# Optimization experiments

Measured on AMD Instinct MI355X. Metric: run time of the kernel, lower is better.

The kernel has to match this reference:

```python
import jax, jax.numpy as jnp
import numpy as np
from jax import lax

B, N = 16, 2048
S0, S1, K = 256, 128, 32
EPS = 1e-5


def bn_relu(x, gamma, beta, axes):
    # training-mode BatchNorm (batch statistics) + ReLU; channel is last dim
    mean = jnp.mean(x, axis=axes, keepdims=True)
    var = jnp.var(x, axis=axes, keepdims=True)
    return jax.nn.relu((x - mean) * lax.rsqrt(var + EPS) * gamma + beta)


def fps(coords, s):
    # farthest point sampling, deterministic start at index 0. coords [B,N,3]
    b, n, _ = coords.shape
    def body(carry, _):
        dist, far = carry
        centroid = jnp.take_along_axis(coords, far[:, None, None], axis=1)  # [B,1,3]
        d = jnp.sum((coords - centroid) ** 2, axis=-1)                      # [B,N]
        dist = jnp.minimum(dist, d)
        return (dist, jnp.argmax(dist, axis=-1).astype(jnp.int32)), far
    init = (jnp.full((b, n), 1e10, coords.dtype), jnp.zeros((b,), jnp.int32))
    _, idx = lax.scan(body, init, None, length=s)
    return jnp.transpose(idx)  # [B,s]


def gather_points(pts, idx):
    # pts [B,N,C], idx [B,...] int -> [B,...,C]
    flat = idx.reshape(idx.shape[0], -1)[..., None]  # [B,M,1]
    out = jnp.take_along_axis(pts, flat, axis=1)     # [B,M,C]
    return out.reshape(*idx.shape, pts.shape[-1])


def sample_and_knn_group(s, k, coords, features):
    # coords [B,N,3], features [B,N,C] -> new_xyz [B,s,3], agg [B,s,k,2C]
    fps_idx = fps(coords, s)
    new_xyz = gather_points(coords, fps_idx)      # [B,s,3]
    center = gather_points(features, fps_idx)     # [B,s,C]
    d2 = jnp.sum((new_xyz[:, :, None, :] - coords[:, None, :, :]) ** 2, axis=-1)  # [B,s,N]
    _, knn_idx = lax.top_k(-d2, k)                # k smallest distances
    grouped = gather_points(features, knn_idx)    # [B,s,k,C]
    agg = jnp.concatenate(
        [grouped - center[:, :, None, :],
         jnp.broadcast_to(center[:, :, None, :], grouped.shape)], axis=-1)
    return new_xyz, agg


def sg_block(coords, features, s, k, w, gamma, beta):
    # conv1x1 -> BN -> ReLU -> max over k neighbors
    new_xyz, nf = sample_and_knn_group(s, k, coords, features)  # nf [B,s,k,d]
    h = jnp.einsum('bskd,od->bsko', nf, w)
    h = bn_relu(h, gamma, beta, axes=(0, 1, 2))
    return new_xyz, jnp.max(h, axis=2)  # [B,s,out]


def setup_inputs() -> dict:
    key = jax.random.key(0)
    ks = jax.random.split(key, 5)
    return {
        'x': jax.random.normal(ks[0], (B, 3, N), jnp.float32),
        'w1': jax.random.normal(ks[1], (64, 3), jnp.float32) * (1.0 / np.sqrt(3)),
        'g1': jnp.ones((64,), jnp.float32), 'b1': jnp.zeros((64,), jnp.float32),
        'w2': jax.random.normal(ks[2], (64, 64), jnp.float32) * 0.125,
        'g2': jnp.ones((64,), jnp.float32), 'b2': jnp.zeros((64,), jnp.float32),
        'w_sg0': jax.random.normal(ks[3], (128, 128), jnp.float32) * (1.0 / np.sqrt(128)),
        'g_sg0': jnp.ones((128,), jnp.float32), 'b_sg0': jnp.zeros((128,), jnp.float32),
        'w_sg1': jax.random.normal(ks[4], (256, 256), jnp.float32) * (1.0 / np.sqrt(256)),
        'g_sg1': jnp.ones((256,), jnp.float32), 'b_sg1': jnp.zeros((256,), jnp.float32),
    }


def reference(x, w1, g1, b1, w2, g2, b2, w_sg0, g_sg0, b_sg0, w_sg1, g_sg1, b_sg1):
    coords = jnp.transpose(x, (0, 2, 1))                   # [B,N,3]
    f = bn_relu(jnp.einsum('bnc,oc->bno', coords, w1), g1, b1, axes=(0, 1))  # [B,N,64]
    f = bn_relu(jnp.einsum('bnc,oc->bno', f, w2), g2, b2, axes=(0, 1))       # [B,N,64]
    xyz1, f1 = sg_block(coords, f, S0, K, w_sg0, g_sg0, b_sg0)   # [B,S0,128]
    _, f2 = sg_block(xyz1, f1, S1, K, w_sg1, g_sg1, b_sg1)       # [B,S1,256]
    return jnp.transpose(f2, (0, 2, 1))                           # [B,256,S1]
```

## Files before the change

kernel.cpp:

```cpp
#include <hip/hip_runtime.h>
#include <float.h>

#define BATCH 16
#define NPTS  2048
#define NS0   256
#define NS1   128
#define KK    32
#define EPSV  1e-5f
#define MROWS 32768.0f

__device__ __forceinline__ float sqdist(float ax,float ay,float az,float bx,float by,float bz){
  float dx=__fsub_rn(ax,bx), dy=__fsub_rn(ay,by), dz=__fsub_rn(az,bz);
  return __fadd_rn(__fadd_rn(__fmul_rn(dx,dx),__fmul_rn(dy,dy)),__fmul_rn(dz,dz));
}

template<int CTRL,int RM>
__device__ __forceinline__ float dpp_fmax_s(float x){
  int t = __builtin_amdgcn_update_dpp((int)0xFF800000, __float_as_int(x), CTRL, RM, 0xf, false);
  return fmaxf(x, __int_as_float(t));
}
template<int CTRL,int RM>
__device__ __forceinline__ float dpp_fmin_s(float x){
  int t = __builtin_amdgcn_update_dpp(0x7F800000, __float_as_int(x), CTRL, RM, 0xf, false);
  return fminf(x, __int_as_float(t));
}
template<int CTRL,int RM>
__device__ __forceinline__ unsigned dpp_umin_s(unsigned x){
  unsigned t = (unsigned)__builtin_amdgcn_update_dpp(-1, (int)x, CTRL, RM, 0xf, false);
  return t<x ? t : x;
}
__device__ __forceinline__ void wave_argmax_f32(float v, unsigned idx, float& mall, int& sel){
  float m=v;
  m=dpp_fmax_s<0x111,0xf>(m); m=dpp_fmax_s<0x112,0xf>(m); m=dpp_fmax_s<0x114,0xf>(m);
  m=dpp_fmax_s<0x118,0xf>(m); m=dpp_fmax_s<0x142,0xa>(m); m=dpp_fmax_s<0x143,0xc>(m);
  mall = __int_as_float(__builtin_amdgcn_readlane(__float_as_int(m),63));
  unsigned c = (v==mall)? idx : 0xFFFFFFFFu;
  c=dpp_umin_s<0x111,0xf>(c); c=dpp_umin_s<0x112,0xf>(c); c=dpp_umin_s<0x114,0xf>(c);
  c=dpp_umin_s<0x118,0xf>(c); c=dpp_umin_s<0x142,0xa>(c); c=dpp_umin_s<0x143,0xc>(c);
  sel = (int)(unsigned)__builtin_amdgcn_readlane((int)c,63);
}
__device__ __forceinline__ int wave_argmin_f32(float v, unsigned idx){
  float m=v;
  m=dpp_fmin_s<0x111,0xf>(m); m=dpp_fmin_s<0x112,0xf>(m); m=dpp_fmin_s<0x114,0xf>(m);
  m=dpp_fmin_s<0x118,0xf>(m); m=dpp_fmin_s<0x142,0xa>(m); m=dpp_fmin_s<0x143,0xc>(m);
  float mall = __int_as_float(__builtin_amdgcn_readlane(__float_as_int(m),63));
  unsigned c = (v==mall)? idx : 0xFFFFFFFFu;
  c=dpp_umin_s<0x111,0xf>(c); c=dpp_umin_s<0x112,0xf>(c); c=dpp_umin_s<0x114,0xf>(c);
  c=dpp_umin_s<0x118,0xf>(c); c=dpp_umin_s<0x142,0xa>(c); c=dpp_umin_s<0x143,0xc>(c);
  return (int)(unsigned)__builtin_amdgcn_readlane((int)c,63);
}


__device__ void embed1_body(int bid, const float* __restrict__ x, const float* __restrict__ w1,
                            float* __restrict__ coords, float* __restrict__ t1){
  __shared__ float w[192];
  __shared__ float xs[3][64];
  __shared__ float fin[64][65];
  int tid = threadIdx.x;
  if (tid < 192) w[tid] = w1[tid];
  int base = bid*64;
  int b = base / NPTS, n0 = base % NPTS;
  if (tid < 192){
    int ch = tid>>6, i = tid&63;
    xs[ch][i] = x[((size_t)b*3+ch)*NPTS + n0 + i];
  }
  __syncthreads();
  if (tid < 64){
    coords[(size_t)(base+tid)*3+0]=xs[0][tid];
    coords[(size_t)(base+tid)*3+1]=xs[1][tid];
    coords[(size_t)(base+tid)*3+2]=xs[2][tid];
  }
  int p = tid>>2, c0 = (tid&3)<<4;
  float cx=xs[0][p], cy=xs[1][p], cz=xs[2][p];
  #pragma unroll
  for(int j=0;j<16;j++){
    int c = c0+j;
    fin[p][c] = cx*w[c*3+0] + cy*w[c*3+1] + cz*w[c*3+2];
  }
  __syncthreads();
  for(int i=tid;i<4096;i+=256){
    int pp=i>>6, c=i&63;
    t1[(size_t)base*64 + i] = fin[pp][c];
  }
}

__device__ void wt_body(int gid, const float* __restrict__ w0, float* __restrict__ wt0,
                        const float* __restrict__ w1, float* __restrict__ wt1){
  if(gid < 128*128){
    int o = gid % 128, c = gid / 128;
    wt0[gid] = w0[o*128 + c];
  } else {
    int g2 = gid - 128*128;
    if(g2 >= 256*256) return;
    int o = g2 % 256, c = g2 / 256;
    wt1[g2] = w1[o*256 + c];
  }
}

__device__ void statsA_body(int blk, const float* __restrict__ t,
                            float* __restrict__ accS, float* __restrict__ accQ){
  int c = threadIdx.x;
  int r0 = blk*128;
  float s=0.f, q=0.f;
  for(int r=0;r<128;r++){
    float v = t[(size_t)(r0+r)*64 + c];
    s+=v; q+=v*v;
  }
  atomicAdd(accS+c, s);
  atomicAdd(accQ+c, q);
}

__device__ void embed2_body(int bid, const float* __restrict__ t1, const float* __restrict__ w2,
                            const float* __restrict__ accS, const float* __restrict__ accQ,
                            const float* __restrict__ g1, const float* __restrict__ b1,
                            float* __restrict__ t2, char* smem){
  float (*fin)[64] = (float(*)[64])smem;
  float* sm = (float*)smem + 4096;
  float* sr = sm+64; float* sg = sr+64; float* sb = sg+64;
  int tid = threadIdx.x;
  if (tid<64){
    float S=accS[tid], Q=accQ[tid];
    float m = S/MROWS, v = Q/MROWS - m*m; if(v<0.f) v=0.f;
    sm[tid]=m; sr[tid]=rsqrtf(v+EPSV); sg[tid]=g1[tid]; sb[tid]=b1[tid];
  }
  __syncthreads();
  int base = bid*64;
  for(int i=tid;i<4096;i+=256){
    int p=i>>6, c=i&63;
    float v = t1[(size_t)(base+p)*64 + c];
    v = (v - sm[c])*sr[c]*sg[c] + sb[c];
    fin[p][c] = v>0.f ? v : 0.f;
  }
  __syncthreads();
  int o = tid & 63, p0 = tid>>6;
  float acc[16];
  #pragma unroll
  for(int i=0;i<16;i++) acc[i]=0.f;
  for(int cc=0; cc<64; cc+=4){
    float4 wv = *(const float4*)(w2 + o*64 + cc);
    #pragma unroll
    for(int i=0;i<16;i++){
      float4 f4 = *(const float4*)&fin[p0 + i*4][cc];
      acc[i] += f4.x*wv.x + f4.y*wv.y + f4.z*wv.z + f4.w*wv.w;
    }
  }
  #pragma unroll
  for(int i=0;i<16;i++) t2[(size_t)(base+p0+i*4)*64 + o] = acc[i];
}

template<int P, int S, int T>
__device__ void fps_body(int b, const float* __restrict__ x, int* __restrict__ outIdx,
                         float* __restrict__ outXyz, char* smem){
  constexpr int PPT = P/T;
  constexpr int NW  = T/64;
  float* sx=(float*)smem; float* sy=sx+P; float* sz=sy+P;
  int* sidx=(int*)(sz+P);
  unsigned long long* rv64=(unsigned long long*)(sidx+S);
  int tid = threadIdx.x;
  const float* xb = x + (size_t)b*3*P;
  float px[PPT], py[PPT], pz[PPT], dist[PPT];
  #pragma unroll
  for(int i=0;i<PPT;i++){
    int n = i*T + tid;
    float X=xb[n], Y=xb[P+n], Z=xb[2*P+n];
    px[i]=X; py[i]=Y; pz[i]=Z; dist[i]=1e10f;
    sx[n]=X; sy[n]=Y; sz[n]=Z;
  }
  __syncthreads();
  int cur = 0;
  float cx=sx[0], cy=sy[0], cz=sz[0];
  for(int s=0;s<S;s++){
    if(tid==0) sidx[s]=cur;
    if(s==S-1) break;
    float bv=-FLT_MAX; int bi=0;
    #pragma unroll
    for(int i=0;i<PPT;i++){
      float d = sqdist(px[i],py[i],pz[i],cx,cy,cz);
      float nd = fminf(dist[i], d);
      dist[i]=nd;
      int n = i*T + tid;
      if(nd>bv){ bv=nd; bi=n; }
    }
    float mall; int sel;
    wave_argmax_f32(bv,(unsigned)bi,mall,sel);
    int sl = s & 1;
    if((tid&63)==0) rv64[sl*NW+(tid>>6)] = ((unsigned long long)__float_as_uint(mall)<<32)|(unsigned)(~sel);
    __syncthreads();
    unsigned long long wk = rv64[sl*NW];
    #pragma unroll
    for(int w=1;w<NW;w++){ unsigned long long t = rv64[sl*NW+w]; if(t>wk) wk=t; }
    cur = (int)(~(unsigned)wk);
    cx=sx[cur]; cy=sy[cur]; cz=sz[cur];
  }
  __syncthreads();
  for(int i=tid; i<S; i+=T){
    int id = sidx[i];
    outIdx[b*S+i] = id;
    outXyz[((size_t)b*S+i)*3+0] = sx[id];
    outXyz[((size_t)b*S+i)*3+1] = sy[id];
    outXyz[((size_t)b*S+i)*3+2] = sz[id];
  }
}

template<int P, int S>
__device__ void fps_wave_body(int b, const float* __restrict__ pts, int* __restrict__ outIdx,
                              float* __restrict__ outXyz, char* smem){
  constexpr int PPT = P/64;
  float4* sp = (float4*)smem;
  int* sidx = (int*)(smem + P*sizeof(float4));
  int lane = threadIdx.x;
  const float* p = pts + (size_t)b*P*3;
  float px[PPT], py[PPT], pz[PPT], dist[PPT];
  #pragma unroll
  for(int i=0;i<PPT;i++){
    int n = i*64 + lane;
    float X=p[n*3], Y=p[n*3+1], Z=p[n*3+2];
    px[i]=X; py[i]=Y; pz[i]=Z; dist[i]=1e10f;
    sp[n] = make_float4(X,Y,Z,0.f);
  }
  __syncthreads();
  int cur = 0;
  float cx=sp[0].x, cy=sp[0].y, cz=sp[0].z;
  for(int s=0;s<S;s++){
    if(lane==0) sidx[s]=cur;
    if(s==S-1) break;
    float bv=-FLT_MAX; int bi=0;
    #pragma unroll
    for(int i=0;i<PPT;i++){
      float d = sqdist(px[i],py[i],pz[i],cx,cy,cz);
      float nd = fminf(dist[i], d);
      dist[i]=nd;
      int n = i*64 + lane;
      if(nd>bv){ bv=nd; bi=n; }
    }
    float mall; int sel;
    wave_argmax_f32(bv,(unsigned)bi,mall,sel);
    cur = sel;
    float4 cp = sp[cur];
    cx=cp.x; cy=cp.y; cz=cp.z;
  }
  __syncthreads();
  for(int i=lane; i<S; i+=64){
    int id = sidx[i];
    float4 cp = sp[id];
    outIdx[b*S+i] = id;
    outXyz[((size_t)b*S+i)*3+0] = cp.x;
    outXyz[((size_t)b*S+i)*3+1] = cp.y;
    outXyz[((size_t)b*S+i)*3+2] = cp.z;
  }
}

template<int P>
__device__ void knn_body(int bq, const float* __restrict__ pts, const float* __restrict__ q,
                         int S, int* __restrict__ knn){
  constexpr int E = P/64;
  int lane = threadIdx.x;
  int b = bq / S;
  const float* p = pts + (size_t)b*P*3;
  float qx=q[(size_t)bq*3], qy=q[(size_t)bq*3+1], qz=q[(size_t)bq*3+2];
  float dl[E];
  float mv = FLT_MAX; unsigned mi = 0xFFFFFFFFu;
  #pragma unroll
  for(int i=0;i<E;i++){
    int n = i*64 + lane;
    float v = sqdist(qx,qy,qz,p[n*3],p[n*3+1],p[n*3+2]);
    dl[i] = v;
    if(v<mv){ mv=v; mi=(unsigned)n; }
  }
  for(int j=0;j<KK;j++){
    int sel = wave_argmin_f32(mv, mi);
    if(lane==0) knn[(size_t)bq*KK+j] = sel;
    if((sel & 63) == lane){
      int slot = sel >> 6;
      #pragma unroll
      for(int i=0;i<E;i++) if(i==slot) dl[i]=FLT_MAX;
      mv = FLT_MAX; mi = 0xFFFFFFFFu;
      #pragma unroll
      for(int i=0;i<E;i++){
        int n=i*64+lane;
        if(dl[i]<mv){ mv=dl[i]; mi=(unsigned)n; }
      }
    }
  }
}

template<int C, int P, bool BN>
__device__ void pass1_body(int bq, const float* __restrict__ feats, const int* __restrict__ knn,
                           const int* __restrict__ fpsIdx, const float* __restrict__ WT,
                           float* __restrict__ hmax, float* __restrict__ hmin,
                           float* __restrict__ part, int S,
                           const float* __restrict__ accS, const float* __restrict__ accQ,
                           const float* __restrict__ bg, const float* __restrict__ bb){
  constexpr int O   = 2*C;
  constexpr int TPB = C;
  constexpr int C4  = C/4;
  constexpr int OG  = O/8;
  constexpr int LDC = C+4;
  __shared__ __align__(16) float gfp[KK*LDC];
  __shared__ __align__(16) float cf[C];
  __shared__ __align__(16) float sa[BN?C:1], sbb[BN?C:1];
  __shared__ float sct[O];
  int tid = threadIdx.x;
  int b = bq / S;
  const float* fb = feats + (size_t)b*P*C;
  int ci = fpsIdx[bq];
  const float* cfg = fb + (size_t)ci*C;
  if(BN){
    float S_=accS[tid], Q_=accQ[tid];
    float m = S_/MROWS, vv = Q_/MROWS - m*m; if(vv<0.f) vv=0.f;
    float a = rsqrtf(vv+EPSV)*bg[tid];
    float sh = bb[tid] - m*a;
    sa[tid]=a; sbb[tid]=sh;
    float cv = a*cfg[tid] + sh;
    cf[tid] = cv>0.f ? cv : 0.f;
    __syncthreads();
  } else {
    cf[tid] = cfg[tid];
  }
  for(int i=tid; i<KK*C4; i+=TPB){
    int k = i/C4, d4 = i - k*C4;
    float4 g = ((const float4*)(fb + (size_t)knn[(size_t)bq*KK+k]*C))[d4];
    float4 r;
    if(BN){
      float4 a4 = *(const float4*)&sa[d4*4];
      float4 s4 = *(const float4*)&sbb[d4*4];
      float4 c4 = *(const float4*)&cf[d4*4];
      float gx = a4.x*g.x+s4.x; gx = gx>0.f?gx:0.f;
      float gy = a4.y*g.y+s4.y; gy = gy>0.f?gy:0.f;
      float gz = a4.z*g.z+s4.z; gz = gz>0.f?gz:0.f;
      float gw = a4.w*g.w+s4.w; gw = gw>0.f?gw:0.f;
      r.x=gx-c4.x; r.y=gy-c4.y; r.z=gz-c4.z; r.w=gw-c4.w;
    } else {
      float4 c4 = ((const float4*)cfg)[d4];
      r.x=g.x-c4.x; r.y=g.y-c4.y; r.z=g.z-c4.z; r.w=g.w-c4.w;
    }
    *(float4*)&gfp[k*LDC + d4*4] = r;
  }
  __syncthreads();
  {
    int o2 = tid*2;
    float ct0=0.f, ct1=0.f;
    for(int c=0;c<C;c+=4){
      float4 c4 = *(const float4*)&cf[c];
      #pragma unroll
      for(int t=0;t<4;t++){
        float cv = ((const float*)&c4)[t];
        float2 wh = *(const float2*)&WT[(size_t)(C+c+t)*O + o2];
        ct0 += cv*wh.x; ct1 += cv*wh.y;
      }
    }
    sct[o2]=ct0; sct[o2+1]=ct1;
  }
  __syncthreads();
  int kg = tid / OG;
  int og = tid % OG;
  float acc[8][8];
  #pragma unroll
  for(int a=0;a<8;a++)
    #pragma unroll
    for(int bb2=0;bb2<8;bb2++) acc[a][bb2]=0.f;
  for(int dc=0; dc<C4; dc++){
    float4 g4[8];
    #pragma unroll
    for(int jk=0;jk<8;jk++) g4[jk] = *(const float4*)&gfp[(kg*8+jk)*LDC + dc*4];
    #pragma unroll
    for(int t=0;t<4;t++){
      const float* wrow = WT + (size_t)(dc*4+t)*O + og*8;
      float4 wa = *(const float4*)wrow;
      float4 wb = *(const float4*)(wrow+4);
      #pragma unroll
      for(int jk=0;jk<8;jk++){
        float gs = ((const float*)&g4[jk])[t];
        acc[jk][0] += gs*wa.x; acc[jk][1] += gs*wa.y; acc[jk][2] += gs*wa.z; acc[jk][3] += gs*wa.w;
        acc[jk][4] += gs*wb.x; acc[jk][5] += gs*wb.y; acc[jk][6] += gs*wb.z; acc[jk][7] += gs*wb.w;
      }
    }
  }
  float tmx[8],tmn[8],tsm[8],tsq[8];
  #pragma unroll
  for(int jo=0;jo<8;jo++){
    int o = og*8+jo;
    float ct = sct[o];
    float s=0.f,q=0.f,mx=-FLT_MAX,mn=FLT_MAX;
    #pragma unroll
    for(int jk=0;jk<8;jk++){
      float h = acc[jk][jo] + ct;
      s+=h; q+=h*h; mx=fmaxf(mx,h); mn=fminf(mn,h);
    }
    tmx[jo]=mx; tmn[jo]=mn; tsm[jo]=s; tsq[jo]=q;
  }
  if constexpr (TPB==64){
    #pragma unroll
    for(int jo=0;jo<8;jo++){
      tmx[jo]=fmaxf(tmx[jo],__shfl_xor(tmx[jo],16)); tmx[jo]=fmaxf(tmx[jo],__shfl_xor(tmx[jo],32));
      tmn[jo]=fminf(tmn[jo],__shfl_xor(tmn[jo],16)); tmn[jo]=fminf(tmn[jo],__shfl_xor(tmn[jo],32));
      tsm[jo]+=__shfl_xor(tsm[jo],16); tsm[jo]+=__shfl_xor(tsm[jo],32);
      tsq[jo]+=__shfl_xor(tsq[jo],16); tsq[jo]+=__shfl_xor(tsq[jo],32);
    }
    if(tid<OG){
      #pragma unroll
      for(int jo=0;jo<8;jo++){
        int o = tid*8+jo;
        hmax[(size_t)bq*O+o]=tmx[jo]; hmin[(size_t)bq*O+o]=tmn[jo];
        part[(size_t)bq*2*O+o]=tsm[jo]; part[(size_t)bq*2*O+O+o]=tsq[jo];
      }
    }
  } else {
    #pragma unroll
    for(int jo=0;jo<8;jo++){
      tmx[jo]=fmaxf(tmx[jo],__shfl_xor(tmx[jo],32));
      tmn[jo]=fminf(tmn[jo],__shfl_xor(tmn[jo],32));
      tsm[jo]+=__shfl_xor(tsm[jo],32);
      tsq[jo]+=__shfl_xor(tsq[jo],32);
    }
    int wv = tid>>6;
    if((tid&63)<32){
      int og_ = tid&31;
      size_t rb = (size_t)bq*2 + wv;
      #pragma unroll
      for(int jo=0;jo<8;jo++){
        int o = og_*8+jo;
        hmax[rb*O+o]=tmx[jo]; hmin[rb*O+o]=tmn[jo];
        part[rb*2*O+o]=tsm[jo]; part[rb*2*O+O+o]=tsq[jo];
      }
    }
  }
}


__global__ __launch_bounds__(256) void k_embed1_wt(const float* __restrict__ x, const float* __restrict__ w1,
                         float* __restrict__ coords, float* __restrict__ t1,
                         const float* __restrict__ wsg0, float* __restrict__ wt0,
                         const float* __restrict__ wsg1, float* __restrict__ wt1,
                         float* __restrict__ accz){
  if(blockIdx.x < 512) embed1_body(blockIdx.x, x, w1, coords, t1);
  else if(blockIdx.x < 832) wt_body((blockIdx.x-512)*256 + threadIdx.x, wsg0, wt0, wsg1, wt1);
  else {
    int tid = threadIdx.x;
    accz[tid]=0.f; accz[tid+256]=0.f; accz[tid+512]=0.f; accz[tid+768]=0.f;
  }
}

__global__ __launch_bounds__(64) void k_statsA(const float* __restrict__ t,
                         float* __restrict__ accS, float* __restrict__ accQ){
  statsA_body(blockIdx.x, t, accS, accQ);
}

__global__ __launch_bounds__(256, 1) void k_fps0_embed2(const float* __restrict__ x,
                         int* __restrict__ fps0, float* __restrict__ xyz0,
                         const float* __restrict__ t1, const float* __restrict__ w2,
                         const float* __restrict__ acc1S, const float* __restrict__ acc1Q,
                         const float* __restrict__ g1, const float* __restrict__ b1,
                         float* __restrict__ t2){
  extern __shared__ char smem[];
  if(blockIdx.x < BATCH) fps_body<NPTS,NS0,256>(blockIdx.x, x, fps0, xyz0, smem);
  else embed2_body(blockIdx.x-BATCH, t1, w2, acc1S, acc1Q, g1, b1, t2, smem);
}

__global__ __launch_bounds__(64, 4) void k_fps1_knn0_st2(const float* __restrict__ xyz0,
                         int* __restrict__ fps1, float* __restrict__ xyz1,
                         const float* __restrict__ coords, int* __restrict__ knn0,
                         const float* __restrict__ t2,
                         float* __restrict__ acc2S, float* __restrict__ acc2Q){
  extern __shared__ char smem[];
  if(blockIdx.x < BATCH) fps_wave_body<NS0,NS1>(blockIdx.x, xyz0, fps1, xyz1, smem);
  else if(blockIdx.x < BATCH + BATCH*NS0) knn_body<NPTS>(blockIdx.x-BATCH, coords, xyz0, NS0, knn0);
  else statsA_body(blockIdx.x - (BATCH + BATCH*NS0), t2, acc2S, acc2Q);
}

__global__ __launch_bounds__(64, 2) void k_pass1a_knn1(const float* __restrict__ t2,
                         const int* __restrict__ knn0, const int* __restrict__ fps0,
                         const float* __restrict__ wt0,
                         float* __restrict__ hmax0, float* __restrict__ hmin0, float* __restrict__ part0,
                         const float* __restrict__ acc2S, const float* __restrict__ acc2Q,
                         const float* __restrict__ g2, const float* __restrict__ b2,
                         const float* __restrict__ xyz0, const float* __restrict__ xyz1,
                         int* __restrict__ knn1){
  if(blockIdx.x < BATCH*NS0)
    pass1_body<64,NPTS,true>(blockIdx.x, t2, knn0, fps0, wt0, hmax0, hmin0, part0, NS0,
                             acc2S, acc2Q, g2, b2);
  else
    knn_body<NS0>(blockIdx.x-BATCH*NS0, xyz0, xyz1, NS1, knn1);
}

__global__ __launch_bounds__(128, 2) void k_pass1b(const float* __restrict__ f1,
                         const int* __restrict__ knn1, const int* __restrict__ fps1,
                         const float* __restrict__ wt1,
                         float* __restrict__ hmax1, float* __restrict__ hmin1, float* __restrict__ part1){
  pass1_body<128,NS0,false>(blockIdx.x, f1, knn1, fps1, wt1, hmax1, hmin1, part1, NS1,
                            nullptr, nullptr, nullptr, nullptr);
}

__global__ __launch_bounds__(256) void k_statsB(const float* __restrict__ part, int W,
                                                float* __restrict__ acc){
  int tid = threadIdx.x;
  int r0 = blockIdx.x*64;
  for(int c=tid; c<W; c+=256){
    float a=0.f;
    for(int r=0;r<64;r++) a += part[(size_t)(r0+r)*W + c];
    atomicAdd(acc+c, a);
  }
}

__global__ __launch_bounds__(256) void k_postmax0(const float* __restrict__ hmax, const float* __restrict__ hmin,
        const float* __restrict__ aS, const float* __restrict__ aQ,
        const float* __restrict__ g, const float* __restrict__ bb, float* __restrict__ f1){
  __shared__ float ssc[128], ssh[128];
  int tid = threadIdx.x;
  if(tid<128){
    float M = (float)(BATCH*NS0*KK);
    float m = aS[tid]/M, v = aQ[tid]/M - m*m; if(v<0.f) v=0.f;
    float sc = rsqrtf(v+EPSV)*g[tid];
    ssc[tid]=sc; ssh[tid]=bb[tid]-m*sc;
  }
  __syncthreads();
  int idx = blockIdx.x*256 + tid;
  int o = idx & 127;
  float sc=ssc[o];
  float h = (sc>=0.f) ? hmax[idx] : hmin[idx];
  float v = h*sc + ssh[o];
  f1[idx] = v>0.f ? v : 0.f;
}

__global__ __launch_bounds__(256) void k_post1tr(const float* __restrict__ hmax, const float* __restrict__ hmin,
        const float* __restrict__ aS, const float* __restrict__ aQ,
        const float* __restrict__ g, const float* __restrict__ bb, float* __restrict__ out){
  __shared__ float ssc[64], ssh[64];
  __shared__ float tile[64][129];
  int tid = threadIdx.x;
  int blk = blockIdx.x; int b = blk>>2; int c0 = (blk&3)*64;
  if(tid<64){
    int o = c0+tid;
    float M = (float)(BATCH*NS1*KK);
    float m = aS[o]/M, v = aQ[o]/M - m*m; if(v<0.f) v=0.f;
    float sc = rsqrtf(v+EPSV)*g[o];
    ssc[tid]=sc; ssh[tid]=bb[o]-m*sc;
  }
  __syncthreads();
  for(int i=tid; i<128*64; i+=256){
    int r=i>>6, ch=i&63;
    size_t rb = (size_t)(b*NS1+r)*2;
    float sc = ssc[ch];
    float va = hmax[rb*256 + c0+ch], vb = hmax[(rb+1)*256 + c0+ch];
    float wa = hmin[rb*256 + c0+ch], wb = hmin[(rb+1)*256 + c0+ch];
    float h = (sc>=0.f) ? fmaxf(va,vb) : fminf(wa,wb);
    float v = h*sc + ssh[ch];
    tile[ch][r] = v>0.f ? v : 0.f;
  }
  __syncthreads();
  for(int i=tid; i<64*128; i+=256){
    int ch=i>>7, s=i&127;
    out[(size_t)b*(256*NS1) + (size_t)(c0+ch)*NS1 + s] = tile[ch][s];
  }
}

extern "C" void kernel_launch(void* const* d_in, const int* in_sizes, int n_in,
                              void* d_out, int out_size, void* d_ws, size_t ws_size,
                              hipStream_t stream){
  const float* x    = (const float*)d_in[0];
  const float* w1   = (const float*)d_in[1];
  const float* g1   = (const float*)d_in[2];
  const float* b1   = (const float*)d_in[3];
  const float* w2   = (const float*)d_in[4];
  const float* g2   = (const float*)d_in[5];
  const float* b2   = (const float*)d_in[6];
  const float* wsg0 = (const float*)d_in[7];
  const float* gsg0 = (const float*)d_in[8];
  const float* bsg0 = (const float*)d_in[9];
  const float* wsg1 = (const float*)d_in[10];
  const float* gsg1 = (const float*)d_in[11];
  const float* bsg1 = (const float*)d_in[12];
  float* out = (float*)d_out;

  float* wsf = (float*)d_ws;
  float* coords = wsf;                    wsf += BATCH*NPTS*3;
  float* t1     = wsf;                    wsf += BATCH*NPTS*64;
  float* t2     = wsf;                    wsf += BATCH*NPTS*64;
  float* acc1S=wsf; wsf+=64;  float* acc1Q=wsf; wsf+=64;
  float* acc2S=wsf; wsf+=64;  float* acc2Q=wsf; wsf+=64;
  float* accB0=wsf; wsf+=256;
  float* accB1=wsf; wsf+=512;
  int*   fps0 = (int*)wsf;                wsf += BATCH*NS0;
  float* xyz0 = wsf;                      wsf += BATCH*NS0*3;
  int*   knn0 = (int*)wsf;                wsf += BATCH*NS0*KK;
  float* hmax0= wsf;                      wsf += BATCH*NS0*128;
  float* hmin0= wsf;                      wsf += BATCH*NS0*128;
  float* part0= wsf;                      wsf += BATCH*NS0*2*128;
  float* f1   = wsf;                      wsf += BATCH*NS0*128;
  int*   fps1 = (int*)wsf;                wsf += BATCH*NS1;
  float* xyz1 = wsf;                      wsf += BATCH*NS1*3;
  int*   knn1 = (int*)wsf;                wsf += BATCH*NS1*KK;
  float* wt0  = wsf;                      wsf += 128*128;
  float* wt1  = wsf;                      wsf += 256*256;
  float* part1 = t1;
  float* hmax1 = t2;
  float* hmin1 = t2 + BATCH*NS1*2*256;

  const int DYN_L3 = (NPTS*3 + NS0)*4 + 2*4*8;
  const int DYN_L4 = NS0*16 + NS1*4;

  k_embed1_wt<<<dim3(833), dim3(256), 0, stream>>>(x, w1, coords, t1, wsg0, wt0, wsg1, wt1, acc1S);
  k_statsA<<<dim3(256), dim3(64), 0, stream>>>(t1, acc1S, acc1Q);
  k_fps0_embed2<<<dim3(BATCH+512), dim3(256), DYN_L3, stream>>>(x, fps0, xyz0,
                                                  t1, w2, acc1S, acc1Q, g1, b1, t2);
  k_fps1_knn0_st2<<<dim3(BATCH + BATCH*NS0 + 256), dim3(64), DYN_L4, stream>>>(
                                                  xyz0, fps1, xyz1, coords, knn0, t2, acc2S, acc2Q);
  k_pass1a_knn1<<<dim3(BATCH*NS0 + BATCH*NS1), dim3(64), 0, stream>>>(t2, knn0, fps0, wt0,
                                                  hmax0, hmin0, part0,
                                                  acc2S, acc2Q, g2, b2,
                                                  xyz0, xyz1, knn1);
  k_statsB<<<dim3(64), dim3(256), 0, stream>>>(part0, 256, accB0);
  k_postmax0<<<dim3(2048), dim3(256), 0, stream>>>(hmax0, hmin0, accB0, accB0+128, gsg0, bsg0, f1);
  k_pass1b<<<dim3(BATCH*NS1), dim3(128), 0, stream>>>(f1, knn1, fps1, wt1, hmax1, hmin1, part1);
  k_statsB<<<dim3(64), dim3(256), 0, stream>>>(part1, 512, accB1);
  k_post1tr<<<dim3(64), dim3(256), 0, stream>>>(hmax1, hmin1, accB1, accB1+256, gsg1, bsg1, out);
}
```

Baseline: 410.3 us.

## Fuse BN statistics into producers and fold postmax BN into pass1b gather

Result: no change. 416.2 us (+1.4%).

```diff
diff --git a/kernel.cpp b/kernel.cpp
--- a/kernel.cpp
+++ b/kernel.cpp
@@ -8,6 +8,8 @@
 #define KK    32
 #define EPSV  1e-5f
 #define MROWS 32768.0f
+#define M0F   131072.0f
+#define M1F   65536.0f
 
 __device__ __forceinline__ float sqdist(float ax,float ay,float az,float bx,float by,float bz){
   float dx=__fsub_rn(ax,bx), dy=__fsub_rn(ay,by), dz=__fsub_rn(az,bz);
@@ -52,12 +54,15 @@
 
 
 __device__ void embed1_body(int bid, const float* __restrict__ x, const float* __restrict__ w1,
-                            float* __restrict__ coords, float* __restrict__ t1){
+                            float* __restrict__ coords, float* __restrict__ t1,
+                            float* __restrict__ acc1S, float* __restrict__ acc1Q,
+                            float* ls, float* lq){
   __shared__ float w[192];
   __shared__ float xs[3][64];
   __shared__ float fin[64][65];
   int tid = threadIdx.x;
   if (tid < 192) w[tid] = w1[tid];
+  if (tid < 64){ ls[tid]=0.f; lq[tid]=0.f; }
   int base = bid*64;
   int b = base / NPTS, n0 = base % NPTS;
   if (tid < 192){
@@ -78,10 +83,17 @@
     fin[p][c] = cx*w[c*3+0] + cy*w[c*3+1] + cz*w[c*3+2];
   }
   __syncthreads();
+  float s=0.f,q=0.f;
   for(int i=tid;i<4096;i+=256){
     int pp=i>>6, c=i&63;
-    t1[(size_t)base*64 + i] = fin[pp][c];
-  }
+    float v = fin[pp][c];
+    t1[(size_t)base*64 + i] = v;
+    s+=v; q+=v*v;
+  }
+  atomicAdd(&ls[tid&63], s);
+  atomicAdd(&lq[tid&63], q);
+  __syncthreads();
+  if(tid<64){ atomicAdd(acc1S+tid, ls[tid]); atomicAdd(acc1Q+tid, lq[tid]); }
 }
 
 __device__ void wt_body(int gid, const float* __restrict__ w0, float* __restrict__ wt0,
@@ -97,23 +109,12 @@
   }
 }
 
-__device__ void statsA_body(int blk, const float* __restrict__ t,
-                            float* __restrict__ accS, float* __restrict__ accQ){
-  int c = threadIdx.x;
-  int r0 = blk*128;
-  float s=0.f, q=0.f;
-  for(int r=0;r<128;r++){
-    float v = t[(size_t)(r0+r)*64 + c];
-    s+=v; q+=v*v;
-  }
-  atomicAdd(accS+c, s);
-  atomicAdd(accQ+c, q);
-}
-
 __device__ void embed2_body(int bid, const float* __restrict__ t1, const float* __restrict__ w2,
                             const float* __restrict__ accS, const float* __restrict__ accQ,
                             const float* __restrict__ g1, const float* __restrict__ b1,
-                            float* __restrict__ t2, char* smem){
+                            float* __restrict__ t2,
+                            float* __restrict__ acc2S, float* __restrict__ acc2Q,
+                            float* ls, float* lq, char* smem){
   float (*fin)[64] = (float(*)[64])smem;
   float* sm = (float*)smem + 4096;
   float* sr = sm+64; float* sg = sr+64; float* sb = sg+64;
@@ -122,6 +123,7 @@
     float S=accS[tid], Q=accQ[tid];
     float m = S/MROWS, v = Q/MROWS - m*m; if(v<0.f) v=0.f;
     sm[tid]=m; sr[tid]=rsqrtf(v+EPSV); sg[tid]=g1[tid]; sb[tid]=b1[tid];
+    ls[tid]=0.f; lq[tid]=0.f;
   }
   __syncthreads();
   int base = bid*64;
@@ -144,8 +146,17 @@
       acc[i] += f4.x*wv.x + f4.y*wv.y + f4.z*wv.z + f4.w*wv.w;
     }
   }
-  #pragma unroll
-  for(int i=0;i<16;i++) t2[(size_t)(base+p0+i*4)*64 + o] = acc[i];
+  float s=0.f,q=0.f;
+  #pragma unroll
+  for(int i=0;i<16;i++){
+    float v = acc[i];
+    t2[(size_t)(base+p0+i*4)*64 + o] = v;
+    s+=v; q+=v*v;
+  }
+  atomicAdd(&ls[o], s);
+  atomicAdd(&lq[o], q);
+  __syncthreads();
+  if(tid<64){ atomicAdd(acc2S+tid, ls[tid]); atomicAdd(acc2Q+tid, lq[tid]); }
 }
 
 template<int P, int S, int T>
@@ -284,8 +295,9 @@
   }
 }
 
-template<int C, int P, bool BN>
-__device__ void pass1_body(int bq, const float* __restrict__ feats, const int* __restrict__ knn,
+template<int C, int P, int MODE>
+__device__ void pass1_body(int bq, const float* __restrict__ feats, const float* __restrict__ feats2,
+                           const int* __restrict__ knn,
                            const int* __restrict__ fpsIdx, const float* __restrict__ WT,
                            float* __restrict__ hmax, float* __restrict__ hmin,
                            float* __restrict__ part, int S,
@@ -298,41 +310,48 @@
   constexpr int LDC = C+4;
   __shared__ __align__(16) float gfp[KK*LDC];
   __shared__ __align__(16) float cf[C];
-  __shared__ __align__(16) float sa[BN?C:1], sbb[BN?C:1];
+  __shared__ __align__(16) float sa[C], sbb[C];
   __shared__ float sct[O];
   int tid = threadIdx.x;
   int b = bq / S;
   const float* fb = feats + (size_t)b*P*C;
+  const float* fb2 = (MODE==2) ? feats2 + (size_t)b*P*C : nullptr;
   int ci = fpsIdx[bq];
-  const float* cfg = fb + (size_t)ci*C;
-  if(BN){
+  {
+    float Mv = (MODE==1) ? MROWS : M0F;
     float S_=accS[tid], Q_=accQ[tid];
-    float m = S_/MROWS, vv = Q_/MROWS - m*m; if(vv<0.f) vv=0.f;
+    float m = S_/Mv, vv = Q_/Mv - m*m; if(vv<0.f) vv=0.f;
     float a = rsqrtf(vv+EPSV)*bg[tid];
     float sh = bb[tid] - m*a;
     sa[tid]=a; sbb[tid]=sh;
-    float cv = a*cfg[tid] + sh;
+    float raw;
+    if(MODE==1) raw = fb[(size_t)ci*C + tid];
+    else        raw = (a>=0.f) ? fb[(size_t)ci*C + tid] : fb2[(size_t)ci*C + tid];
+    float cv = a*raw + sh;
     cf[tid] = cv>0.f ? cv : 0.f;
-    __syncthreads();
-  } else {
-    cf[tid] = cfg[tid];
-  }
+  }
+  __syncthreads();
   for(int i=tid; i<KK*C4; i+=TPB){
     int k = i/C4, d4 = i - k*C4;
-    float4 g = ((const float4*)(fb + (size_t)knn[(size_t)bq*KK+k]*C))[d4];
+    size_t row = (size_t)knn[(size_t)bq*KK+k]*C;
+    float4 a4 = *(const float4*)&sa[d4*4];
+    float4 s4 = *(const float4*)&sbb[d4*4];
+    float4 c4 = *(const float4*)&cf[d4*4];
+    float4 g  = ((const float4*)(fb + row))[d4];
     float4 r;
-    if(BN){
-      float4 a4 = *(const float4*)&sa[d4*4];
-      float4 s4 = *(const float4*)&sbb[d4*4];
-      float4 c4 = *(const float4*)&cf[d4*4];
+    if(MODE==2){
+      float4 g2 = ((const float4*)(fb2 + row))[d4];
+      float gx = (a4.x>=0.f? g.x : g2.x)*a4.x + s4.x; gx = gx>0.f?gx:0.f;
+      float gy = (a4.y>=0.f? g.y : g2.y)*a4.y + s4.y; gy = gy>0.f?gy:0.f;
+      float gz = (a4.z>=0.f? g.z : g2.z)*a4.z + s4.z; gz = gz>0.f?gz:0.f;
+      float gw = (a4.w>=0.f? g.w : g2.w)*a4.w + s4.w; gw = gw>0.f?gw:0.f;
+      r.x=gx-c4.x; r.y=gy-c4.y; r.z=gz-c4.z; r.w=gw-c4.w;
+    } else {
       float gx = a4.x*g.x+s4.x; gx = gx>0.f?gx:0.f;
       float gy = a4.y*g.y+s4.y; gy = gy>0.f?gy:0.f;
       float gz = a4.z*g.z+s4.z; gz = gz>0.f?gz:0.f;
       float gw = a4.w*g.w+s4.w; gw = gw>0.f?gw:0.f;
       r.x=gx-c4.x; r.y=gy-c4.y; r.z=gz-c4.z; r.w=gw-c4.w;
-    } else {
-      float4 c4 = ((const float4*)cfg)[d4];
-      r.x=g.x-c4.x; r.y=g.y-c4.y; r.z=g.z-c4.z; r.w=g.w-c4.w;
     }
     *(float4*)&gfp[k*LDC + d4*4] = r;
   }
@@ -432,18 +451,10 @@
                          float* __restrict__ coords, float* __restrict__ t1,
                          const float* __restrict__ wsg0, float* __restrict__ wt0,
                          const float* __restrict__ wsg1, float* __restrict__ wt1,
-                         float* __restrict__ accz){
-  if(blockIdx.x < 512) embed1_body(blockIdx.x, x, w1, coords, t1);
-  else if(blockIdx.x < 832) wt_body((blockIdx.x-512)*256 + threadIdx.x, wsg0, wt0, wsg1, wt1);
-  else {
-    int tid = threadIdx.x;
-    accz[tid]=0.f; accz[tid+256]=0.f; accz[tid+512]=0.f; accz[tid+768]=0.f;
-  }
-}
-
-__global__ __launch_bounds__(64) void k_statsA(const float* __restrict__ t,
-                         float* __restrict__ accS, float* __restrict__ accQ){
-  statsA_body(blockIdx.x, t, accS, accQ);
+                         float* __restrict__ acc1S, float* __restrict__ acc1Q){
+  __shared__ float ls[64], lq[64];
+  if(blockIdx.x < 512) embed1_body(blockIdx.x, x, w1, coords, t1, acc1S, acc1Q, ls, lq);
+  else wt_body((blockIdx.x-512)*256 + threadIdx.x, wsg0, wt0, wsg1, wt1);
 }
 
 __global__ __launch_bounds__(256, 1) void k_fps0_embed2(const float* __restrict__ x,
@@ -451,21 +462,20 @@
                          const float* __restrict__ t1, const float* __restrict__ w2,
                          const float* __restrict__ acc1S, const float* __restrict__ acc1Q,
                          const float* __restrict__ g1, const float* __restrict__ b1,
-                         float* __restrict__ t2){
-  extern __shared__ char smem[];
-  if(blockIdx.x < BATCH) fps_body<NPTS,NS0,256>(blockIdx.x, x, fps0, xyz0, smem);
-  else embed2_body(blockIdx.x-BATCH, t1, w2, acc1S, acc1Q, g1, b1, t2, smem);
-}
-
-__global__ __launch_bounds__(64, 4) void k_fps1_knn0_st2(const float* __restrict__ xyz0,
-                         int* __restrict__ fps1, float* __restrict__ xyz1,
-                         const float* __restrict__ coords, int* __restrict__ knn0,
-                         const float* __restrict__ t2,
+                         float* __restrict__ t2,
                          float* __restrict__ acc2S, float* __restrict__ acc2Q){
   extern __shared__ char smem[];
-  if(blockIdx.x < BATCH) fps_wave_body<NS0,NS1>(blockIdx.x, xyz0, fps1, xyz1, smem);
-  else if(blockIdx.x < BATCH + BATCH*NS0) knn_body<NPTS>(blockIdx.x-BATCH, coords, xyz0, NS0, knn0);
-  else statsA_body(blockIdx.x - (BATCH + BATCH*NS0), t2, acc2S, acc2Q);
+  __shared__ float ls[64], lq[64];
+  if(blockIdx.x < BATCH) fps_body<NPTS,NS0,256>(blockIdx.x, x, fps0, xyz0, smem);
+  else embed2_body(blockIdx.x-BATCH, t1, w2, acc1S, acc1Q, g1, b1, t2, acc2S, acc2Q, ls, lq, smem);
+}
+
+__global__ __launch_bounds__(64, 4) void k_fps1_knn0(const float* __restrict__ xyz0,
+                         int* __restrict__ fps1, float* __restrict__ xyz1,
+                         const float* __restrict__ coords, int* __restrict__ knn0){
+  extern __shared__ char smem[];
+  if(blockIdx.x < BATCH) fps_wave_body<NS0,NS1>(blockIdx.x, xyz0, fps1, fps1 ? xyz1 : xyz1, smem);
+  else knn_body<NPTS>(blockIdx.x-BATCH, coords, xyz0, NS0, knn0);
 }
 
 __global__ __launch_bounds__(64, 2) void k_pass1a_knn1(const float* __restrict__ t2,
@@ -477,18 +487,21 @@
                          const float* __restrict__ xyz0, const float* __restrict__ xyz1,
                          int* __restrict__ knn1){
   if(blockIdx.x < BATCH*NS0)
-    pass1_body<64,NPTS,true>(blockIdx.x, t2, knn0, fps0, wt0, hmax0, hmin0, part0, NS0,
-                             acc2S, acc2Q, g2, b2);
+    pass1_body<64,NPTS,1>(blockIdx.x, t2, nullptr, knn0, fps0, wt0, hmax0, hmin0, part0, NS0,
+                          acc2S, acc2Q, g2, b2);
   else
     knn_body<NS0>(blockIdx.x-BATCH*NS0, xyz0, xyz1, NS1, knn1);
 }
 
-__global__ __launch_bounds__(128, 2) void k_pass1b(const float* __restrict__ f1,
+__global__ __launch_bounds__(128, 2) void k_pass1b(const float* __restrict__ hmax0,
+                         const float* __restrict__ hmin0,
                          const int* __restrict__ knn1, const int* __restrict__ fps1,
                          const float* __restrict__ wt1,
-                         float* __restrict__ hmax1, float* __restrict__ hmin1, float* __restrict__ part1){
-  pass1_body<128,NS0,false>(blockIdx.x, f1, knn1, fps1, wt1, hmax1, hmin1, part1, NS1,
-                            nullptr, nullptr, nullptr, nullptr);
+                         float* __restrict__ hmax1, float* __restrict__ hmin1, float* __restrict__ part1,
+                         const float* __restrict__ accB0S, const float* __restrict__ accB0Q,
+                         const float* __restrict__ gsg0, const float* __restrict__ bsg0){
+  pass1_body<128,NS0,2>(blockIdx.x, hmax0, hmin0, knn1, fps1, wt1, hmax1, hmin1, part1, NS1,
+                        accB0S, accB0Q, gsg0, bsg0);
 }
 
 __global__ __launch_bounds__(256) void k_statsB(const float* __restrict__ part, int W,
@@ -500,26 +513,6 @@
     for(int r=0;r<64;r++) a += part[(size_t)(r0+r)*W + c];
     atomicAdd(acc+c, a);
   }
-}
-
-__global__ __launch_bounds__(256) void k_postmax0(const float* __restrict__ hmax, const float* __restrict__ hmin,
-        const float* __restrict__ aS, const float* __restrict__ aQ,
-        const float* __restrict__ g, const float* __restrict__ bb, float* __restrict__ f1){
-  __shared__ float ssc[128], ssh[128];
-  int tid = threadIdx.x;
-  if(tid<128){
-    float M = (float)(BATCH*NS0*KK);
-    float m = aS[tid]/M, v = aQ[tid]/M - m*m; if(v<0.f) v=0.f;
-    float sc = rsqrtf(v+EPSV)*g[tid];
-    ssc[tid]=sc; ssh[tid]=bb[tid]-m*sc;
-  }
-  __syncthreads();
-  int idx = blockIdx.x*256 + tid;
-  int o = idx & 127;
-  float sc=ssc[o];
-  float h = (sc>=0.f) ? hmax[idx] : hmin[idx];
-  float v = h*sc + ssh[o];
-  f1[idx] = v>0.f ? v : 0.f;
 }
 
 __global__ __launch_bounds__(256) void k_post1tr(const float* __restrict__ hmax, const float* __restrict__ hmin,
@@ -531,8 +524,7 @@
   int blk = blockIdx.x; int b = blk>>2; int c0 = (blk&3)*64;
   if(tid<64){
     int o = c0+tid;
-    float M = (float)(BATCH*NS1*KK);
-    float m = aS[o]/M, v = aQ[o]/M - m*m; if(v<0.f) v=0.f;
+    float m = aS[o]/M1F, v = aQ[o]/M1F - m*m; if(v<0.f) v=0.f;
     float sc = rsqrtf(v+EPSV)*g[o];
     ssc[tid]=sc; ssh[tid]=bb[o]-m*sc;
   }
@@ -586,7 +578,6 @@
   float* hmax0= wsf;                      wsf += BATCH*NS0*128;
   float* hmin0= wsf;                      wsf += BATCH*NS0*128;
   float* part0= wsf;                      wsf += BATCH*NS0*2*128;
-  float* f1   = wsf;                      wsf += BATCH*NS0*128;
   int*   fps1 = (int*)wsf;                wsf += BATCH*NS1;
   float* xyz1 = wsf;                      wsf += BATCH*NS1*3;
   int*   knn1 = (int*)wsf;                wsf += BATCH*NS1*KK;
@@ -599,19 +590,20 @@
   const int DYN_L3 = (NPTS*3 + NS0)*4 + 2*4*8;
   const int DYN_L4 = NS0*16 + NS1*4;
 
-  k_embed1_wt<<<dim3(833), dim3(256), 0, stream>>>(x, w1, coords, t1, wsg0, wt0, wsg1, wt1, acc1S);
-  k_statsA<<<dim3(256), dim3(64), 0, stream>>>(t1, acc1S, acc1Q);
+  hipMemsetAsync(acc1S, 0, 1024*sizeof(float), stream);
+  k_embed1_wt<<<dim3(832), dim3(256), 0, stream>>>(x, w1, coords, t1, wsg0, wt0, wsg1, wt1,
+                                                   acc1S, acc1Q);
   k_fps0_embed2<<<dim3(BATCH+512), dim3(256), DYN_L3, stream>>>(x, fps0, xyz0,
-                                                  t1, w2, acc1S, acc1Q, g1, b1, t2);
-  k_fps1_knn0_st2<<<dim3(BATCH + BATCH*NS0 + 256), dim3(64), DYN_L4, stream>>>(
-                                                  xyz0, fps1, xyz1, coords, knn0, t2, acc2S, acc2Q);
+                                                  t1, w2, acc1S, acc1Q, g1, b1, t2, acc2S, acc2Q);
+  k_fps1_knn0<<<dim3(BATCH + BATCH*NS0), dim3(64), DYN_L4, stream>>>(xyz0, fps1, xyz1, coords, knn0);
   k_pass1a_knn1<<<dim3(BATCH*NS0 + BATCH*NS1), dim3(64), 0, stream>>>(t2, knn0, fps0, wt0,
                                                   hmax0, hmin0, part0,
                                                   acc2S, acc2Q, g2, b2,
                                                   xyz0, xyz1, knn1);
   k_statsB<<<dim3(64), dim3(256), 0, stream>>>(part0, 256, accB0);
-  k_postmax0<<<dim3(2048), dim3(256), 0, stream>>>(hmax0, hmin0, accB0, accB0+128, gsg0, bsg0, f1);
-  k_pass1b<<<dim3(BATCH*NS1), dim3(128), 0, stream>>>(f1, knn1, fps1, wt1, hmax1, hmin1, part1);
+  k_pass1b<<<dim3(BATCH*NS1), dim3(128), 0, stream>>>(hmax0, hmin0, knn1, fps1, wt1,
+                                                  hmax1, hmin1, part1,
+                                                  accB0, accB0+128, gsg0, bsg0);
   k_statsB<<<dim3(64), dim3(256), 0, stream>>>(part1, 512, accB1);
   k_post1tr<<<dim3(64), dim3(256), 0, stream>>>(hmax1, hmin1, accB1, accB1+256, gsg1, bsg1, out);
 }
```
